# Performance work log

Hardware: AMD Instinct MI355X
Metric: run time of the kernel (lower is better)

## Reference

```python
import jax, jax.numpy as jnp
import numpy as np

D, NH, NL, NP, DFF = 256, 8, 4, 4, 1024
HD = D // NH
SHAPES = np.array([[64, 64], [32, 32], [16, 16], [8, 8]], dtype=np.int32)  # (H, W) per level


def _layer_norm(x, g, b, eps=1e-5):
    mu = jnp.mean(x, -1, keepdims=True)
    var = jnp.mean((x - mu) ** 2, -1, keepdims=True)
    return (x - mu) * jax.lax.rsqrt(var + eps) * g + b


def _bilinear_sample(value_l, loc):
    # value_l: (N, H, W, NH, HD); loc: (N, Lq, NH, NP, 2) normalized to [0,1]
    # Matches F.grid_sample(align_corners=False, padding_mode='zeros') on grid 2*loc-1.
    N, H, W = value_l.shape[0], value_l.shape[1], value_l.shape[2]
    x = loc[..., 0] * W - 0.5
    y = loc[..., 1] * H - 0.5
    x0 = jnp.floor(x)
    y0 = jnp.floor(y)
    wx1 = x - x0
    wy1 = y - y0
    b_idx = jnp.arange(N)[:, None, None, None]
    h_idx = jnp.arange(NH)[None, None, :, None]

    def gather(yi, xi):
        valid = (yi >= 0) & (yi < H) & (xi >= 0) & (xi < W)
        yc = jnp.clip(yi, 0, H - 1).astype(jnp.int32)
        xc = jnp.clip(xi, 0, W - 1).astype(jnp.int32)
        v = value_l[b_idx, yc, xc, h_idx]  # (N, Lq, NH, NP, HD)
        return v * valid[..., None].astype(value_l.dtype)

    v00 = gather(y0, x0)
    v01 = gather(y0, x0 + 1)
    v10 = gather(y0 + 1, x0)
    v11 = gather(y0 + 1, x0 + 1)
    wx1 = wx1[..., None]
    wy1 = wy1[..., None]
    top = v00 * (1 - wx1) + v01 * wx1
    bot = v10 * (1 - wx1) + v11 * wx1
    return top * (1 - wy1) + bot * wy1  # (N, Lq, NH, NP, HD)


def setup_inputs() -> dict:
    key = jax.random.key(0)
    ks = jax.random.split(key, 24)
    N, Lq = 8, int(SHAPES.prod(axis=1).sum())  # 5440
    s = 0.02
    return {
        "src": jax.random.normal(ks[0], (N, Lq, D), jnp.float32),
        "pos": jax.random.normal(ks[1], (N, Lq, D), jnp.float32),
        "reference_points": jax.random.uniform(ks[2], (N, Lq, NL, 2), jnp.float32),
        "spatial_shapes": jnp.asarray(SHAPES),
        "W_value": s * jax.random.normal(ks[3], (D, D)),
        "b_value": jnp.zeros((D,)),
        "W_off": s * jax.random.normal(ks[4], (D, NH * NL * NP * 2)),
        "b_off": 0.5 * jax.random.normal(ks[5], (NH * NL * NP * 2,)),
        "W_attn": s * jax.random.normal(ks[6], (D, NH * NL * NP)),
        "b_attn": jnp.zeros((NH * NL * NP,)),
        "W_out": s * jax.random.normal(ks[7], (D, D)),
        "b_out": jnp.zeros((D,)),
        "ln1_g": jnp.ones((D,)),
        "ln1_b": jnp.zeros((D,)),
        "W1": s * jax.random.normal(ks[8], (D, DFF)),
        "b1": jnp.zeros((DFF,)),
        "W2": s * jax.random.normal(ks[9], (DFF, D)),
        "b2": jnp.zeros((D,)),
        "ln2_g": jnp.ones((D,)),
        "ln2_b": jnp.zeros((D,)),
    }


def reference(src, pos, reference_points, spatial_shapes,
              W_value, b_value, W_off, b_off, W_attn, b_attn, W_out, b_out,
              ln1_g, ln1_b, W1, b1, W2, b2, ln2_g, ln2_b):
    shapes = np.asarray(spatial_shapes)  # static (NL, 2)
    N, Lq = src.shape[0], src.shape[1]

    # --- MSDeformAttn ---
    query = src + pos
    value = (src @ W_value + b_value).reshape(N, Lq, NH, HD)
    offsets = (query @ W_off + b_off).reshape(N, Lq, NH, NL, NP, 2)
    attn = jax.nn.softmax((query @ W_attn + b_attn).reshape(N, Lq, NH, NL * NP), axis=-1)
    attn = attn.reshape(N, Lq, NH, NL, NP)
    # offset normalizer is (W, H) per level
    norm = jnp.asarray(np.stack([shapes[:, 1], shapes[:, 0]], -1), jnp.float32)  # (NL, 2)
    loc = reference_points[:, :, None, :, None, :] + offsets / norm[None, None, None, :, None, :]

    out = jnp.zeros((N, Lq, NH, HD), src.dtype)
    start = 0
    for l in range(NL):
        H, W = int(shapes[l, 0]), int(shapes[l, 1])
        v_l = jax.lax.dynamic_slice_in_dim(value, start, H * W, axis=1).reshape(N, H, W, NH, HD)
        sampled = _bilinear_sample(v_l, loc[:, :, :, l])  # (N, Lq, NH, NP, HD)
        out = out + jnp.einsum('nqhp,nqhpd->nqhd', attn[:, :, :, l], sampled)
        start += H * W
    src2 = out.reshape(N, Lq, D) @ W_out + b_out

    # --- residual + norm + FFN (dropout=0, eval) ---
    x = _layer_norm(src + src2, ln1_g, ln1_b)
    ffn = jax.nn.relu(x @ W1 + b1) @ W2 + b2
    return _layer_norm(x + ffn, ln2_g, ln2_b)
```

## Files before the change

kernel.cpp:

```cpp
#include <hip/hip_runtime.h>
#include <math.h>

#define LQ_ 5440
#define NB_ 8
#define NQ_ (NB_ * LQ_)
#define D_  256
#define NH_ 8
#define HD_ 32

typedef __attribute__((ext_vector_type(8))) short short8;
typedef __attribute__((ext_vector_type(4))) float f32x4;

__device__ __forceinline__ ushort f2bf(float f) {
    union { float f; unsigned u; } v; v.f = f;
    unsigned u = v.u;
    unsigned r = (u + 0x7FFFu + ((u >> 16) & 1u)) >> 16;
    return (ushort)r;
}
__device__ __forceinline__ float bf2f(ushort u) {
    union { unsigned u; float f; } v; v.u = ((unsigned)u) << 16; return v.f;
}

__device__ __forceinline__ void gload_lds16(const void* g, void* l) {
    __builtin_amdgcn_global_load_lds(
        (const __attribute__((address_space(1))) void*)g,
        (__attribute__((address_space(3))) void*)l, 16, 0, 0);
}

__device__ __forceinline__ void wg_barrier() {
    __builtin_amdgcn_sched_barrier(0);
    __builtin_amdgcn_s_barrier();
    __builtin_amdgcn_sched_barrier(0);
}

__device__ __forceinline__ int xcd_swz(int flat, int nwg) {
    const int xc  = flat & 7;
    const int sl  = flat >> 3;
    const int q8  = nwg >> 3;
    const int rm8 = nwg & 7;
    return (xc < rm8 ? xc * (q8 + 1) : rm8 * (q8 + 1) + (xc - rm8) * q8) + sl;
}

#define TPREP_ 736

__global__ __launch_bounds__(256)
void prep(const float* __restrict__ src, const float* __restrict__ pos,
          ushort* __restrict__ s_bf, ushort* __restrict__ q_bf,
          const float* __restrict__ Wv, const float* __restrict__ Woff,
          const float* __restrict__ Wattn, const float* __restrict__ Wout,
          const float* __restrict__ W1, const float* __restrict__ W2,
          ushort* __restrict__ Wv_t, ushort* __restrict__ Woff_t,
          ushort* __restrict__ Wattn_t, ushort* __restrict__ Wout_t,
          ushort* __restrict__ W1_t, ushort* __restrict__ W2_t) {
    __shared__ float tile[32][33];
    const int bid = blockIdx.x;
    const int tid = threadIdx.x;

    if (bid >= TPREP_) {
        const int i = (bid - TPREP_) * 256 + tid;
        const float4 s = ((const float4*)src)[i];
        const float4 p = ((const float4*)pos)[i];
        ushort4 a, b;
        a.x = f2bf(s.x); a.y = f2bf(s.y); a.z = f2bf(s.z); a.w = f2bf(s.w);
        b.x = f2bf(s.x + p.x); b.y = f2bf(s.y + p.y);
        b.z = f2bf(s.z + p.z); b.w = f2bf(s.w + p.w);
        ((ushort4*)s_bf)[i] = a;
        ((ushort4*)q_bf)[i] = b;
        return;
    }

    const float* W; ushort* Wt; int K, N, bx, by;
    if (bid < 64)       { W = Wv;    Wt = Wv_t;    K = 256;  N = 256;  bx = bid % 8;         by = bid / 8; }
    else if (bid < 128) { W = Woff;  Wt = Woff_t;  K = 256;  N = 256;  bx = (bid-64) % 8;    by = (bid-64) / 8; }
    else if (bid < 160) { W = Wattn; Wt = Wattn_t; K = 256;  N = 128;  bx = (bid-128) % 4;   by = (bid-128) / 4; }
    else if (bid < 224) { W = Wout;  Wt = Wout_t;  K = 256;  N = 256;  bx = (bid-160) % 8;   by = (bid-160) / 8; }
    else if (bid < 480) { W = W1;    Wt = W1_t;    K = 256;  N = 1024; bx = (bid-224) % 32;  by = (bid-224) / 32; }
    else                { W = W2;    Wt = W2_t;    K = 1024; N = 256;  bx = (bid-480) % 8;   by = (bid-480) / 8; }

    const int tx = tid & 31;
    const int ty = tid >> 5;
    for (int i = ty; i < 32; i += 8)
        tile[i][tx] = W[(size_t)(by * 32 + i) * N + bx * 32 + tx];
    __syncthreads();
    for (int i = ty; i < 32; i += 8)
        Wt[(size_t)(bx * 32 + i) * K + by * 32 + tx] = f2bf(tile[tx][i]);
}

#define BM 128
#define BN 128
#define BK 64

__device__ __forceinline__ void gemm_body(
    ushort* __restrict__ lAb, ushort* __restrict__ lBb,
    const ushort* __restrict__ A, const ushort* __restrict__ Bt,
    const float* __restrict__ bias, float* __restrict__ Cf,
    ushort* __restrict__ Cb, int N, int K, int relu, int col0, int row0) {
    const int t    = threadIdx.x;
    const int w    = t >> 6;
    const int lr   = t & 15;
    const int quad = (t >> 4) & 3;
    const int wm   = (w >> 1) * 64;
    const int wn   = (w & 1) * 64;

    f32x4 acc[4][4];
    #pragma unroll
    for (int i = 0; i < 4; ++i)
        #pragma unroll
        for (int j = 0; j < 4; ++j)
            acc[i][j] = (f32x4){0.f, 0.f, 0.f, 0.f};

    const int sr = t >> 3;
    const int sc = (t & 7) * 8;
    const size_t aoff = (size_t)(row0 + sr) * K + sc;
    const size_t boff = (size_t)(col0 + sr) * K + sc;
    const int wb = w * 1024;

    auto stage = [&](int buf, int k0) {
        char* la = (char*)(lAb + buf * (BM * BK)) + wb;
        char* lb = (char*)(lBb + buf * (BN * BK)) + wb;
        #pragma unroll
        for (int g = 0; g < 4; ++g) {
            gload_lds16(A  + aoff + k0 + (size_t)g * 32 * K, la + g * 4096);
            gload_lds16(Bt + boff + k0 + (size_t)g * 32 * K, lb + g * 4096);
        }
    };

    stage(0, 0);
    int cur = 0;
    for (int k0 = 0; k0 < K; k0 += BK) {
        if (k0 + BK < K) {
            stage(cur ^ 1, k0 + BK);
            asm volatile("s_waitcnt vmcnt(8)" ::: "memory");
        } else {
            asm volatile("s_waitcnt vmcnt(0)" ::: "memory");
        }
        wg_barrier();
        const ushort* pA = lAb + cur * (BM * BK);
        const ushort* pB = lBb + cur * (BN * BK);
        #pragma unroll
        for (int kk = 0; kk < 2; ++kk) {
            short8 af[4], bfr[4];
            #pragma unroll
            for (int i = 0; i < 4; ++i)
                af[i] = *(const short8*)(pA + (wm + i * 16 + lr) * BK + kk * 32 + quad * 8);
            #pragma unroll
            for (int j = 0; j < 4; ++j)
                bfr[j] = *(const short8*)(pB + (wn + j * 16 + lr) * BK + kk * 32 + quad * 8);
            #pragma unroll
            for (int i = 0; i < 4; ++i)
                #pragma unroll
                for (int j = 0; j < 4; ++j)
                    acc[i][j] = __builtin_amdgcn_mfma_f32_16x16x32_bf16(af[i], bfr[j], acc[i][j], 0, 0, 0);
        }
        wg_barrier();
        cur ^= 1;
    }

    #pragma unroll
    for (int j = 0; j < 4; ++j) {
        const int col = col0 + wn + j * 16 + lr;
        const float bb = bias ? bias[col] : 0.f;
        #pragma unroll
        for (int i = 0; i < 4; ++i) {
            const int rbase = row0 + wm + i * 16 + quad * 4;
            #pragma unroll
            for (int r = 0; r < 4; ++r) {
                float v = acc[i][j][r] + bb;
                if (relu) v = fmaxf(v, 0.f);
                if (Cf) Cf[(size_t)(rbase + r) * N + col] = v;
                else    Cb[(size_t)(rbase + r) * N + col] = f2bf(v);
            }
        }
    }
}

__global__ __launch_bounds__(256)
void mfma_gemm(const ushort* __restrict__ A, const ushort* __restrict__ Bt,
               const float* __restrict__ bias, float* __restrict__ Cf,
               ushort* __restrict__ Cb, int N, int K, int relu) {
    __shared__ ushort lA[2][BM * BK];
    __shared__ ushort lB[2][BN * BK];
    const int nt  = gridDim.x;
    const int wi  = xcd_swz(blockIdx.y * nt + blockIdx.x, nt * gridDim.y);
    gemm_body(&lA[0][0], &lB[0][0], A, Bt, bias, Cf, Cb, N, K, relu,
              (wi % nt) * BN, (wi / nt) * BM);
}

__global__ __launch_bounds__(256)
void gemm_vc(const ushort* __restrict__ s_bf, const ushort* __restrict__ q_bf,
             const ushort* __restrict__ Wv_t, const ushort* __restrict__ Woff_t,
             const float* __restrict__ b_value,
             ushort* __restrict__ val_bf, ushort* __restrict__ comb_bf) {
    __shared__ ushort lA[2][BM * BK];
    __shared__ ushort lB[2][BN * BK];
    const int wi   = xcd_swz(blockIdx.x, gridDim.x);
    const int ci   = wi % 5;
    const int row0 = (wi / 5) * BM;
    if (ci < 2)
        gemm_body(&lA[0][0], &lB[0][0], s_bf, Wv_t, b_value, nullptr, val_bf,
                  256, 256, 0, ci * BN, row0);
    else
        gemm_body(&lA[0][0], &lB[0][0], q_bf, Woff_t, nullptr, nullptr, comb_bf,
                  384, 256, 0, (ci - 2) * BN, row0);
}

__global__ __launch_bounds__(256)
void msda_sample(const ushort* __restrict__ value, const ushort* __restrict__ comb,
                 const float* __restrict__ b_off, const float* __restrict__ b_attn,
                 const float* __restrict__ refp, ushort* __restrict__ out) {
    __shared__ int   s_addr[256][4];
    __shared__ float s_w[256][4];

    const int t   = threadIdx.x;
    const int tq  = t >> 7;
    const int u   = t & 127;
    const int bid = blockIdx.x;
    const int swz = (bid & 7) * (NQ_ / 2 / 8) + (bid >> 3);
    const int nq  = swz * 2 + tq;
    const int n   = nq / LQ_;

    {
        const int h = u >> 4;
        const int p = u & 15;
        const int l = p >> 2;

        const int starts[4] = {0, 4096, 5120, 5376};
        const int Wl = 64 >> l;

        const float a = bf2f(comb[(size_t)nq * 384 + 256 + u]) + b_attn[u];
        const float e = __expf(a);
        float s = e;
        #pragma unroll
        for (int o = 8; o > 0; o >>= 1) s += __shfl_xor(s, o);
        const float wgt = e * __builtin_amdgcn_rcpf(s);

        const float rx = refp[(size_t)nq * 8 + l * 2 + 0];
        const float ry = refp[(size_t)nq * 8 + l * 2 + 1];
        const uint  opk = *(const uint*)(comb + (size_t)nq * 384 + u * 2);
        const float ox = bf2f((ushort)(opk & 0xffffu)) + b_off[u * 2 + 0];
        const float oy = bf2f((ushort)(opk >> 16))     + b_off[u * 2 + 1];

        union { uint ui; float f; } fwu, rvu;
        fwu.ui = (uint)(133 - l) << 23;
        rvu.ui = (uint)(121 + l) << 23;
        const float fw = fwu.f;
        const float x  = (rx + ox * rvu.f) * fw - 0.5f;
        const float y  = (ry + oy * rvu.f) * fw - 0.5f;
        const float x0f = floorf(x), y0f = floorf(y);
        const int   x0 = (int)x0f, y0 = (int)y0f;
        const float wx1 = x - x0f, wy1 = y - y0f;
        const float wx0 = 1.f - wx1, wy0 = 1.f - wy1;

        const float xm0 = (x0 >= 0 && x0 < Wl) ? 1.f : 0.f;
        const float xm1 = (x0 + 1 >= 0 && x0 + 1 < Wl) ? 1.f : 0.f;
        const float ym0 = (y0 >= 0 && y0 < Wl) ? 1.f : 0.f;
        const float ym1 = (y0 + 1 >= 0 && y0 + 1 < Wl) ? 1.f : 0.f;

        const int x0c = min(max(x0, 0), Wl - 1);
        const int x1c = min(max(x0 + 1, 0), Wl - 1);
        const int y0c = min(max(y0, 0), Wl - 1);
        const int y1c = min(max(y0 + 1, 0), Wl - 1);

        const int base = (n * LQ_ + starts[l]) * 512 + h * 64;
        s_addr[t][0] = base + (y0c * Wl + x0c) * 512;
        s_addr[t][1] = base + (y0c * Wl + x1c) * 512;
        s_addr[t][2] = base + (y1c * Wl + x0c) * 512;
        s_addr[t][3] = base + (y1c * Wl + x1c) * 512;
        s_w[t][0] = wgt * wy0 * wx0 * ym0 * xm0;
        s_w[t][1] = wgt * wy0 * wx1 * ym0 * xm1;
        s_w[t][2] = wgt * wy1 * wx0 * ym1 * xm0;
        s_w[t][3] = wgt * wy1 * wx1 * ym1 * xm1;
    }
    __syncthreads();

    {
        const int h   = u >> 4;
        const int d2  = u & 15;
        const int sb  = tq * 128 + h * 16;
        const uint dby = (uint)(d2 * 4);
        const char* vbase = (const char*)value;

        float acc0 = 0.f, acc1 = 0.f;
        #pragma unroll
        for (int p = 0; p < 16; ++p) {
            const int*   ap = s_addr[sb + p];
            const float* wp = s_w[sb + p];
            #pragma unroll
            for (int c = 0; c < 4; ++c) {
                const uint v = *(const uint*)(vbase + ((uint)ap[c] + dby));
                const float w = wp[c];
                union { uint u; float f; } lo, hi;
                lo.u = v << 16;
                hi.u = v & 0xffff0000u;
                acc0 = fmaf(lo.f, w, acc0);
                acc1 = fmaf(hi.f, w, acc1);
            }
        }
        const uint packed = (uint)f2bf(acc0) | ((uint)f2bf(acc1) << 16);
        ((uint*)out)[(size_t)nq * 128 + u] = packed;
    }
}

__global__ __launch_bounds__(256)
void add_ln(const float* __restrict__ af, const ushort* __restrict__ ab,
            const ushort* __restrict__ b,
            const float* __restrict__ g, const float* __restrict__ be,
            float* __restrict__ outf, ushort* __restrict__ outb) {
    const int row  = blockIdx.x * 4 + (threadIdx.x >> 6);
    const int lane = threadIdx.x & 63;
    const size_t base = (size_t)row * 256 + lane * 4;

    float4 av;
    if (af) {
        av = *(const float4*)(af + base);
    } else {
        const ushort4 a4 = *(const ushort4*)(ab + base);
        av.x = bf2f(a4.x); av.y = bf2f(a4.y); av.z = bf2f(a4.z); av.w = bf2f(a4.w);
    }
    const ushort4 bv = *(const ushort4*)(b + base);
    float4 x;
    x.x = av.x + bf2f(bv.x); x.y = av.y + bf2f(bv.y);
    x.z = av.z + bf2f(bv.z); x.w = av.w + bf2f(bv.w);

    float s = x.x + x.y + x.z + x.w;
    #pragma unroll
    for (int o = 32; o > 0; o >>= 1) s += __shfl_xor(s, o);
    const float mu = s * (1.f / 256.f);

    float4 dx;
    dx.x = x.x - mu; dx.y = x.y - mu; dx.z = x.z - mu; dx.w = x.w - mu;
    float vv = dx.x * dx.x + dx.y * dx.y + dx.z * dx.z + dx.w * dx.w;
    #pragma unroll
    for (int o = 32; o > 0; o >>= 1) vv += __shfl_xor(vv, o);
    const float rstd = rsqrtf(vv * (1.f / 256.f) + 1e-5f);

    const float4 gv  = *(const float4*)(g  + lane * 4);
    const float4 bev = *(const float4*)(be + lane * 4);
    float4 y;
    y.x = dx.x * rstd * gv.x + bev.x;
    y.y = dx.y * rstd * gv.y + bev.y;
    y.z = dx.z * rstd * gv.z + bev.z;
    y.w = dx.w * rstd * gv.w + bev.w;

    if (outf) *(float4*)(outf + base) = y;
    if (outb) {
        ushort4 yb;
        yb.x = f2bf(y.x); yb.y = f2bf(y.y); yb.z = f2bf(y.z); yb.w = f2bf(y.w);
        *(ushort4*)(outb + base) = yb;
    }
}

extern "C" void kernel_launch(void* const* d_in, const int* in_sizes, int n_in,
                              void* d_out, int out_size, void* d_ws, size_t ws_size,
                              hipStream_t stream) {
    const float* src     = (const float*)d_in[0];
    const float* pos     = (const float*)d_in[1];
    const float* refp    = (const float*)d_in[2];
    const float* W_value = (const float*)d_in[4];
    const float* b_value = (const float*)d_in[5];
    const float* W_off   = (const float*)d_in[6];
    const float* b_off   = (const float*)d_in[7];
    const float* W_attn  = (const float*)d_in[8];
    const float* b_attn  = (const float*)d_in[9];
    const float* W_out   = (const float*)d_in[10];
    const float* b_out   = (const float*)d_in[11];
    const float* ln1g    = (const float*)d_in[12];
    const float* ln1b    = (const float*)d_in[13];
    const float* W1      = (const float*)d_in[14];
    const float* b1      = (const float*)d_in[15];
    const float* W2      = (const float*)d_in[16];
    const float* b2      = (const float*)d_in[17];
    const float* ln2g    = (const float*)d_in[18];
    const float* ln2b    = (const float*)d_in[19];
    float* out = (float*)d_out;
    char*  ws  = (char*)d_ws;

    const size_t SZ_BF  = (size_t)NQ_ * 256 * 2;
    const size_t SZ_CB  = (size_t)NQ_ * 384 * 2;
    ushort* s_bf    = (ushort*)(ws);
    ushort* q_bf    = (ushort*)(ws + SZ_BF);
    ushort* val_bf  = (ushort*)(ws + 2 * SZ_BF);
    ushort* comb    = (ushort*)(ws + 3 * SZ_BF);
    ushort* samp_bf = (ushort*)(ws + 3 * SZ_BF + SZ_CB);
    ushort* h_bf    = (ushort*)(ws);
    ushort* x_bf    = (ushort*)(ws + 3 * SZ_BF + SZ_CB);
    char*   wbase   = ws + 3 * SZ_BF + SZ_CB + SZ_BF;
    ushort* Wv_t    = (ushort*)(wbase);
    ushort* Woff_t  = (ushort*)(wbase + 131072);
    ushort* Wattn_t = (ushort*)(wbase + 262144);
    ushort* Wout_t  = (ushort*)(wbase + 327680);
    ushort* W1_t    = (ushort*)(wbase + 458752);
    ushort* W2_t    = (ushort*)(wbase + 983040);
    char*   fbase   = wbase + 1507328;
    ushort* src2b   = (ushort*)(fbase);
    ushort* ffn2b   = src2b;

    prep<<<dim3(TPREP_ + (NQ_ * 256 / 4) / 256), 256, 0, stream>>>(
        src, pos, s_bf, q_bf, W_value, W_off, W_attn, W_out, W1, W2,
        Wv_t, Woff_t, Wattn_t, Wout_t, W1_t, W2_t);

    const int MT = NQ_ / BM;

    gemm_vc<<<dim3(5 * MT), 256, 0, stream>>>(s_bf, q_bf, Wv_t, Woff_t, b_value, val_bf, comb);
    msda_sample<<<dim3(NQ_ / 2), 256, 0, stream>>>(val_bf, comb, b_off, b_attn, refp, samp_bf);
    mfma_gemm<<<dim3(2, MT), 256, 0, stream>>>(samp_bf, Wout_t, b_out, nullptr, src2b, 256, 256, 0);
    add_ln<<<dim3(NQ_ / 4), 256, 0, stream>>>(nullptr, s_bf, src2b, ln1g, ln1b, nullptr, x_bf);
    mfma_gemm<<<dim3(8, MT), 256, 0, stream>>>(x_bf, W1_t, b1, nullptr, h_bf, 1024, 256, 1);
    mfma_gemm<<<dim3(2, MT), 256, 0, stream>>>(h_bf, W2_t, b2, nullptr, ffn2b, 256, 1024, 0);
    add_ln<<<dim3(NQ_ / 4), 256, 0, stream>>>(nullptr, x_bf, ffn2b, ln2g, ln2b, out, nullptr);
}
```

Baseline: 418.3 us.

## Enlarge GEMM row tile to 256 and drop LDS double buffering

Doubles the GEMM block tile in M from 128 to 256, so each wave computes an 8x4 grid of MFMA tiles instead of 4x4. The double-buffered LDS pipeline with manual vmcnt waits is replaced by a single buffer with two __syncthreads per K step, and launch bounds now request 2 blocks per CU. The aim is more A/B reuse per load and lower LDS use to raise occupancy. The cost is that global loads no longer overlap MFMA work, accumulator register pressure doubles, and the grid has half as many blocks.

```diff
diff --git a/kernel.cpp b/kernel.cpp
--- a/kernel.cpp
+++ b/kernel.cpp
@@ -25,12 +25,6 @@
     __builtin_amdgcn_global_load_lds(
         (const __attribute__((address_space(1))) void*)g,
         (__attribute__((address_space(3))) void*)l, 16, 0, 0);
-}
-
-__device__ __forceinline__ void wg_barrier() {
-    __builtin_amdgcn_sched_barrier(0);
-    __builtin_amdgcn_s_barrier();
-    __builtin_amdgcn_sched_barrier(0);
 }
 
 __device__ __forceinline__ int xcd_swz(int flat, int nwg) {
@@ -86,12 +80,12 @@
         Wt[(size_t)(bx * 32 + i) * K + by * 32 + tx] = f2bf(tile[tx][i]);
 }
 
-#define BM 128
+#define BM 256
 #define BN 128
 #define BK 64
 
 __device__ __forceinline__ void gemm_body(
-    ushort* __restrict__ lAb, ushort* __restrict__ lBb,
+    ushort* __restrict__ lA, ushort* __restrict__ lB,
     const ushort* __restrict__ A, const ushort* __restrict__ Bt,
     const float* __restrict__ bias, float* __restrict__ Cf,
     ushort* __restrict__ Cb, int N, int K, int relu, int col0, int row0) {
@@ -99,12 +93,12 @@
     const int w    = t >> 6;
     const int lr   = t & 15;
     const int quad = (t >> 4) & 3;
-    const int wm   = (w >> 1) * 64;
+    const int wm   = (w >> 1) * 128;
     const int wn   = (w & 1) * 64;
 
-    f32x4 acc[4][4];
+    f32x4 acc[8][4];
     #pragma unroll
-    for (int i = 0; i < 4; ++i)
+    for (int i = 0; i < 8; ++i)
         #pragma unroll
         for (int j = 0; j < 4; ++j)
             acc[i][j] = (f32x4){0.f, 0.f, 0.f, 0.f};
@@ -115,45 +109,30 @@
     const size_t boff = (size_t)(col0 + sr) * K + sc;
     const int wb = w * 1024;
 
-    auto stage = [&](int buf, int k0) {
-        char* la = (char*)(lAb + buf * (BM * BK)) + wb;
-        char* lb = (char*)(lBb + buf * (BN * BK)) + wb;
-        #pragma unroll
-        for (int g = 0; g < 4; ++g) {
-            gload_lds16(A  + aoff + k0 + (size_t)g * 32 * K, la + g * 4096);
-            gload_lds16(Bt + boff + k0 + (size_t)g * 32 * K, lb + g * 4096);
-        }
-    };
-
-    stage(0, 0);
-    int cur = 0;
     for (int k0 = 0; k0 < K; k0 += BK) {
-        if (k0 + BK < K) {
-            stage(cur ^ 1, k0 + BK);
-            asm volatile("s_waitcnt vmcnt(8)" ::: "memory");
-        } else {
-            asm volatile("s_waitcnt vmcnt(0)" ::: "memory");
-        }
-        wg_barrier();
-        const ushort* pA = lAb + cur * (BM * BK);
-        const ushort* pB = lBb + cur * (BN * BK);
+        __syncthreads();
+        #pragma unroll
+        for (int g = 0; g < 8; ++g)
+            gload_lds16(A + aoff + k0 + (size_t)g * 32 * K, (char*)lA + wb + g * 4096);
+        #pragma unroll
+        for (int g = 0; g < 4; ++g)
+            gload_lds16(Bt + boff + k0 + (size_t)g * 32 * K, (char*)lB + wb + g * 4096);
+        __syncthreads();
         #pragma unroll
         for (int kk = 0; kk < 2; ++kk) {
-            short8 af[4], bfr[4];
-            #pragma unroll
-            for (int i = 0; i < 4; ++i)
-                af[i] = *(const short8*)(pA + (wm + i * 16 + lr) * BK + kk * 32 + quad * 8);
+            short8 af[8], bfr[4];
+            #pragma unroll
+            for (int i = 0; i < 8; ++i)
+                af[i] = *(const short8*)(lA + (wm + i * 16 + lr) * BK + kk * 32 + quad * 8);
             #pragma unroll
             for (int j = 0; j < 4; ++j)
-                bfr[j] = *(const short8*)(pB + (wn + j * 16 + lr) * BK + kk * 32 + quad * 8);
-            #pragma unroll
-            for (int i = 0; i < 4; ++i)
+                bfr[j] = *(const short8*)(lB + (wn + j * 16 + lr) * BK + kk * 32 + quad * 8);
+            #pragma unroll
+            for (int i = 0; i < 8; ++i)
                 #pragma unroll
                 for (int j = 0; j < 4; ++j)
                     acc[i][j] = __builtin_amdgcn_mfma_f32_16x16x32_bf16(af[i], bfr[j], acc[i][j], 0, 0, 0);
         }
-        wg_barrier();
-        cur ^= 1;
     }
 
     #pragma unroll
@@ -161,7 +140,7 @@
         const int col = col0 + wn + j * 16 + lr;
         const float bb = bias ? bias[col] : 0.f;
         #pragma unroll
-        for (int i = 0; i < 4; ++i) {
+        for (int i = 0; i < 8; ++i) {
             const int rbase = row0 + wm + i * 16 + quad * 4;
             #pragma unroll
             for (int r = 0; r < 4; ++r) {
@@ -174,33 +153,33 @@
     }
 }
 
-__global__ __launch_bounds__(256)
+__global__ __launch_bounds__(256, 2)
 void mfma_gemm(const ushort* __restrict__ A, const ushort* __restrict__ Bt,
                const float* __restrict__ bias, float* __restrict__ Cf,
                ushort* __restrict__ Cb, int N, int K, int relu) {
-    __shared__ ushort lA[2][BM * BK];
-    __shared__ ushort lB[2][BN * BK];
+    __shared__ ushort lA[BM * BK];
+    __shared__ ushort lB[BN * BK];
     const int nt  = gridDim.x;
     const int wi  = xcd_swz(blockIdx.y * nt + blockIdx.x, nt * gridDim.y);
-    gemm_body(&lA[0][0], &lB[0][0], A, Bt, bias, Cf, Cb, N, K, relu,
+    gemm_body(lA, lB, A, Bt, bias, Cf, Cb, N, K, relu,
               (wi % nt) * BN, (wi / nt) * BM);
 }
 
-__global__ __launch_bounds__(256)
+__global__ __launch_bounds__(256, 2)
 void gemm_vc(const ushort* __restrict__ s_bf, const ushort* __restrict__ q_bf,
              const ushort* __restrict__ Wv_t, const ushort* __restrict__ Woff_t,
              const float* __restrict__ b_value,
              ushort* __restrict__ val_bf, ushort* __restrict__ comb_bf) {
-    __shared__ ushort lA[2][BM * BK];
-    __shared__ ushort lB[2][BN * BK];
+    __shared__ ushort lA[BM * BK];
+    __shared__ ushort lB[BN * BK];
     const int wi   = xcd_swz(blockIdx.x, gridDim.x);
     const int ci   = wi % 5;
     const int row0 = (wi / 5) * BM;
     if (ci < 2)
-        gemm_body(&lA[0][0], &lB[0][0], s_bf, Wv_t, b_value, nullptr, val_bf,
+        gemm_body(lA, lB, s_bf, Wv_t, b_value, nullptr, val_bf,
                   256, 256, 0, ci * BN, row0);
     else
-        gemm_body(&lA[0][0], &lB[0][0], q_bf, Woff_t, nullptr, nullptr, comb_bf,
+        gemm_body(lA, lB, q_bf, Woff_t, nullptr, nullptr, comb_bf,
                   384, 256, 0, (ci - 2) * BN, row0);
 }
 
```

Result: no change. 418.7 us (+0.1%).
